# Kernel optimization log

Hardware: AMD Instinct MI355X
Metric: run time of the kernel (lower is better)

Reference implementation:

```python
import jax, jax.numpy as jnp
import numpy as np

N_NODES = 100000
N_EDGES = 600000
PRE = 128
NEXT = 128


def setup_inputs() -> dict:
    key = jax.random.key(0)
    k1, k2, k3, k4, k5, k6 = jax.random.split(key, 6)
    node_embedding = jax.random.normal(k1, (N_NODES, PRE), dtype=jnp.float32)
    edges = jax.random.randint(k2, (N_EDGES, 2), 0, N_NODES, dtype=jnp.int64)
    # Linear weights use torch convention [out, in]; scale ~ He-ish for sanity.
    s = 1.0 / np.sqrt(PRE)
    W_left = jax.random.normal(k3, (NEXT, PRE), dtype=jnp.float32) * s
    W_right = jax.random.normal(k4, (NEXT, PRE), dtype=jnp.float32) * s
    W_update = jax.random.normal(k5, (NEXT, PRE), dtype=jnp.float32) * s
    b_update = jax.random.normal(k6, (NEXT,), dtype=jnp.float32) * s
    return {
        "node_embedding": node_embedding,
        "edges": edges,
        "W_left": W_left,
        "W_right": W_right,
        "W_update": W_update,
        "b_update": b_update,
        "next_size": NEXT,
    }


def reference(node_embedding, edges, W_left, W_right, W_update, b_update, next_size):
    # Vectorized form of the per-edge loop:
    #   for each edge (i0, i1):
    #     lg  = sigmoid(W_l @ x[i0])
    #     rg  = sigmoid(W_r @ x[i1])
    #     mid = tanh(W_u @ (x[i0] + x[i1]) + b)
    #     out = lg*mid + rg*mid
    x0 = node_embedding[edges[:, 0]]  # [E, pre]
    x1 = node_embedding[edges[:, 1]]  # [E, pre]
    lg = jax.nn.sigmoid(jnp.einsum("ep,np->en", x0, W_left))
    rg = jax.nn.sigmoid(jnp.einsum("ep,np->en", x1, W_right))
    mid = jnp.tanh(jnp.einsum("ep,np->en", x0 + x1, W_update) + b_update)
    return (lg + rg) * mid  # [E, next]
```

## Files before the change

kernel.cpp:

```cpp
#include <hip/hip_runtime.h>
#include <hip/hip_bf16.h>
#include <hip/hip_fp16.h>

typedef __attribute__((ext_vector_type(8))) short short8;
typedef __attribute__((ext_vector_type(4))) float f32x4;

__device__ __forceinline__ float bflo(unsigned int u) { return __uint_as_float(u << 16); }
__device__ __forceinline__ float bfhi(unsigned int u) { return __uint_as_float(u & 0xffff0000u); }
__device__ __forceinline__ unsigned int bfrne(float f) {
    unsigned int u = __float_as_uint(f);
    return (u + 0x7fffu + ((u >> 16) & 1u)) >> 16;
}
__device__ __forceinline__ unsigned int packbf2(float lo, float hi) {
    return (bfrne(lo) & 0xffffu) | (bfrne(hi) << 16);
}
__device__ __forceinline__ short8 pack8(const float* f) {
    short8 r;
#pragma unroll
    for (int i = 0; i < 8; i += 2) {
        unsigned int p = packbf2(f[i], f[i + 1]);
        r[i] = (short)(p & 0xffffu);
        r[i + 1] = (short)(p >> 16);
    }
    return r;
}
__device__ __forceinline__ void unpackbf8(uint4 v, float* f) {
    const unsigned int* p = (const unsigned int*)&v;
#pragma unroll
    for (int j = 0; j < 4; ++j) { f[2 * j] = bflo(p[j]); f[2 * j + 1] = bfhi(p[j]); }
}

__device__ __forceinline__ unsigned int packh2(float lo, float hi) {
    unsigned int a = __half_as_ushort(__float2half_rn(lo));
    unsigned int b = __half_as_ushort(__float2half_rn(hi));
    return a | (b << 16);
}
__device__ __forceinline__ void unpackh8(uint4 v, float* f) {
    const unsigned int* p = (const unsigned int*)&v;
#pragma unroll
    for (int j = 0; j < 4; ++j) {
        f[2 * j]     = __half2float(__ushort_as_half((unsigned short)(p[j] & 0xffffu)));
        f[2 * j + 1] = __half2float(__ushort_as_half((unsigned short)(p[j] >> 16)));
    }
}

__device__ __forceinline__ float fast_rcp(float x) { return __builtin_amdgcn_rcpf(x); }
__device__ __forceinline__ float sigmoidf_fast(float x) { return fast_rcp(1.0f + __expf(-x)); }
__device__ __forceinline__ float tanhf_fast(float x) {
    float e = __expf(2.0f * x);
    return 1.0f - 2.0f * fast_rcp(e + 1.0f);
}

__global__ void sniff_kernel(const unsigned short* __restrict__ emb,
                             const int* __restrict__ e32, int* __restrict__ flags)
{
    __shared__ int s_f32, s_nz;
    const int t = threadIdx.x;
    if (t == 0) { s_f32 = 0; s_nz = 0; }
    __syncthreads();
    int bad = 0;
#pragma unroll 4
    for (int j = 0; j < 64; ++j) {
        unsigned int u = emb[t * 64 + j];
        if (((u >> 7) & 0xFFu) == 0xFFu) bad = 1;
    }
    int nz = 0;
#pragma unroll
    for (int j = 0; j < 8; ++j)
        if (e32[(t * 8 + j) * 2 + 1] != 0) nz = 1;
    if (bad) atomicOr(&s_f32, 1);
    if (nz) atomicOr(&s_nz, 1);
    __syncthreads();
    if (t == 0) { flags[0] = s_f32; flags[1] = s_nz ? 0 : 1; }
}

__global__ __launch_bounds__(256)
void prep_kernel(const void* __restrict__ w0v, const void* __restrict__ w1v,
                 const void* __restrict__ w2v,
                 unsigned short* __restrict__ Wb, const int* __restrict__ flags)
{
    const int in_f32 = flags[0];
    const int w = blockIdx.x;
    const void* Wv = (w == 0) ? w0v : (w == 1 ? w1v : w2v);
    unsigned short* dst = Wb + w * 16384;
    const int tid = threadIdx.x;
    if (in_f32) {
        const float* W = (const float*)Wv;
#pragma unroll
        for (int it = 0; it < 8; ++it) {
            int i = (tid + it * 256) * 8;
            float f[8];
            *(uint4*)&f[0] = *(const uint4*)(W + i);
            *(uint4*)&f[4] = *(const uint4*)(W + i + 4);
            *(short8*)(dst + i) = pack8(f);
        }
    } else {
        const unsigned short* W = (const unsigned short*)Wv;
#pragma unroll
        for (int it = 0; it < 8; ++it) {
            int i = (tid + it * 256) * 8;
            *(uint4*)(dst + i) = *(const uint4*)(W + i);
        }
    }
}

__global__ __launch_bounds__(256, 2)
void proj_kernel(const void* __restrict__ embv,
                 const unsigned short* __restrict__ Wb,
                 unsigned short* __restrict__ SLp,
                 unsigned short* __restrict__ SRp,
                 unsigned short* __restrict__ Up,
                 const int* __restrict__ flags, int n_nodes)
{
    const int in_f32 = flags[0];
    const int m0 = blockIdx.x * 128;

    __shared__ unsigned short ldsh[128 * 136];
    __shared__ unsigned short ldsl[128 * 136];

    const int tid  = threadIdx.x;
    const int lane = tid & 63;
    const int wave = tid >> 6;
    const int wm   = wave & 1;
    const int wn   = wave >> 1;
    const int l15  = lane & 15;
    const int lgp  = lane >> 4;

    if (in_f32) {
        const float* emb = (const float*)embv;
#pragma unroll
        for (int it = 0; it < 8; ++it) {
            int i = tid + it * 256;
            int row = i >> 4, ch = i & 15;
            int g = m0 + row;
            float f[8] = {0.f, 0.f, 0.f, 0.f, 0.f, 0.f, 0.f, 0.f};
            if (g < n_nodes) {
                const float* src = emb + (size_t)g * 128 + ch * 8;
                *(uint4*)&f[0] = *(const uint4*)src;
                *(uint4*)&f[4] = *(const uint4*)(src + 4);
            }
            short8 h, l;
#pragma unroll
            for (int j = 0; j < 8; ++j) {
                unsigned int uh = bfrne(f[j]);
                h[j] = (short)uh;
                float r = f[j] - __uint_as_float(uh << 16);
                l[j] = (short)bfrne(r);
            }
            *(short8*)(&ldsh[row * 136 + ch * 8]) = h;
            *(short8*)(&ldsl[row * 136 + ch * 8]) = l;
        }
    } else {
        const unsigned short* emb = (const unsigned short*)embv;
#pragma unroll
        for (int it = 0; it < 4; ++it) {
            int i = tid + it * 256;
            int row = i >> 3, ch = i & 7;
            int g = m0 + row;
            uint4 v = make_uint4(0u, 0u, 0u, 0u);
            if (g < n_nodes) v = *(const uint4*)(emb + (size_t)g * 128 + ch * 8);
            *(uint4*)(&ldsh[row * 136 + ch * 8]) = v;
        }
    }

    __syncthreads();

#pragma unroll 1
    for (int w = 0; w < 3; ++w) {
        const unsigned short* Wp = Wb + w * 16384;

        short8 bf[4][4];
#pragma unroll
        for (int nj = 0; nj < 4; ++nj) {
            const unsigned short* wrow = Wp + (size_t)(wn * 64 + nj * 16 + l15) * 128 + lgp * 8;
#pragma unroll
            for (int s = 0; s < 4; ++s)
                bf[s][nj] = *(const short8*)(wrow + s * 32);
        }

        f32x4 acc[4][4];
#pragma unroll
        for (int mi = 0; mi < 4; ++mi)
#pragma unroll
            for (int nj = 0; nj < 4; ++nj)
                acc[mi][nj] = (f32x4){0.f, 0.f, 0.f, 0.f};

#pragma unroll
        for (int s = 0; s < 4; ++s) {
            short8 afh[4];
#pragma unroll
            for (int mi = 0; mi < 4; ++mi)
                afh[mi] = *(const short8*)(&ldsh[(wm * 64 + mi * 16 + l15) * 136 + s * 32 + lgp * 8]);
#pragma unroll
            for (int mi = 0; mi < 4; ++mi)
#pragma unroll
                for (int nj = 0; nj < 4; ++nj)
                    acc[mi][nj] = __builtin_amdgcn_mfma_f32_16x16x32_bf16(
                        afh[mi], bf[s][nj], acc[mi][nj], 0, 0, 0);
            if (in_f32) {
                short8 afl[4];
#pragma unroll
                for (int mi = 0; mi < 4; ++mi)
                    afl[mi] = *(const short8*)(&ldsl[(wm * 64 + mi * 16 + l15) * 136 + s * 32 + lgp * 8]);
#pragma unroll
                for (int mi = 0; mi < 4; ++mi)
#pragma unroll
                    for (int nj = 0; nj < 4; ++nj)
                        acc[mi][nj] = __builtin_amdgcn_mfma_f32_16x16x32_bf16(
                            afl[mi], bf[s][nj], acc[mi][nj], 0, 0, 0);
            }
        }

        unsigned short* out = (w == 0) ? SLp : (w == 1 ? SRp : Up);
        const bool gate = (w < 2);
        const bool odd = (lane & 1);
#pragma unroll
        for (int mi = 0; mi < 4; ++mi) {
            int nodeBase = m0 + wm * 64 + mi * 16 + lgp * 4;
#pragma unroll
            for (int nj = 0; nj < 4; ++nj) {
                float v0 = acc[mi][nj][0];
                float v1 = acc[mi][nj][1];
                float v2 = acc[mi][nj][2];
                float v3 = acc[mi][nj][3];
                if (gate) {
                    v0 = sigmoidf_fast(v0); v1 = sigmoidf_fast(v1);
                    v2 = sigmoidf_fast(v2); v3 = sigmoidf_fast(v3);
                }
                float p0 = __shfl_xor(v0, 1), p1 = __shfl_xor(v1, 1);
                float p2 = __shfl_xor(v2, 1), p3 = __shfl_xor(v3, 1);
                unsigned int pkA, pkB; int rA, rB;
                if (!odd) { pkA = packh2(v0, p0); rA = 0; pkB = packh2(v1, p1); rB = 1; }
                else      { pkA = packh2(p2, v2); rA = 2; pkB = packh2(p3, v3); rB = 3; }
                int colE = wn * 64 + nj * 16 + (l15 & ~1);
                int na = nodeBase + rA, nb = nodeBase + rB;
                if (na < n_nodes) *(unsigned int*)(out + (size_t)na * 128 + colE) = pkA;
                if (nb < n_nodes) *(unsigned int*)(out + (size_t)nb * 128 + colE) = pkB;
            }
        }
    }
}

__global__ __launch_bounds__(256)
void edge_kernel(const int* __restrict__ e32,
                 const unsigned short* __restrict__ SL,
                 const unsigned short* __restrict__ SR,
                 const unsigned short* __restrict__ U,
                 const void* __restrict__ biasv,
                 void* __restrict__ outv,
                 const int* __restrict__ flags, int n_edges)
{
    const int in_f32 = flags[0];
    const int i64    = flags[1];
    const int tid = threadIdx.x;
    const int e = blockIdx.x * 16 + (tid >> 4);
    if (e >= n_edges) return;
    const int c = (tid & 15) * 8;

    int a, b;
    if (i64) { int4 ev = *(const int4*)(e32 + 4 * (size_t)e); a = ev.x; b = ev.z; }
    else     { int2 ev = *(const int2*)(e32 + 2 * (size_t)e); a = ev.x; b = ev.y; }

    float slf[8], srf[8], uaf[8], ubf[8], bif[8];
    unpackh8(*(const uint4*)(SL + (size_t)a * 128 + c), slf);
    unpackh8(*(const uint4*)(SR + (size_t)b * 128 + c), srf);
    unpackh8(*(const uint4*)(U  + (size_t)a * 128 + c), uaf);
    unpackh8(*(const uint4*)(U  + (size_t)b * 128 + c), ubf);
    if (in_f32) {
        const float* bp = (const float*)biasv + c;
        *(uint4*)&bif[0] = *(const uint4*)bp;
        *(uint4*)&bif[4] = *(const uint4*)(bp + 4);
    } else {
        unpackbf8(*(const uint4*)((const unsigned short*)biasv + c), bif);
    }

    float o[8];
#pragma unroll
    for (int j = 0; j < 8; ++j) {
        float s = slf[j] + srf[j];
        float x = uaf[j] + ubf[j] + bif[j];
        o[j] = s * tanhf_fast(x);
    }

    if (in_f32) {
        float* op = (float*)outv + (size_t)e * 128 + c;
        *(uint4*)op = *(const uint4*)&o[0];
        *(uint4*)(op + 4) = *(const uint4*)&o[4];
    } else {
        unsigned int res[4];
#pragma unroll
        for (int j = 0; j < 4; ++j) res[j] = packbf2(o[2 * j], o[2 * j + 1]);
        *(uint4*)((unsigned short*)outv + (size_t)e * 128 + c) = *(const uint4*)res;
    }
}

extern "C" void kernel_launch(void* const* d_in, const int* in_sizes, int n_in,
                              void* d_out, int out_size, void* d_ws, size_t ws_size,
                              hipStream_t stream)
{
    const void* emb   = d_in[0];
    const int*  edges = (const int*)d_in[1];
    const void* Wl    = d_in[2];
    const void* Wr    = d_in[3];
    const void* Wu    = d_in[4];
    const void* bias  = d_in[5];

    const int n_nodes = in_sizes[0] / 128;
    const int n_edges = in_sizes[1] / 2;

    int* flags = (int*)d_ws;
    unsigned short* Wb = (unsigned short*)((char*)d_ws + 256);
    const size_t plane_elems = (size_t)n_nodes * 128;
    unsigned short* SLp = Wb + 3 * 16384;
    unsigned short* SRp = SLp + plane_elems;
    unsigned short* Up  = SRp + plane_elems;

    sniff_kernel<<<1, 256, 0, stream>>>((const unsigned short*)emb, edges, flags);

    prep_kernel<<<3, 256, 0, stream>>>(Wl, Wr, Wu, Wb, flags);

    dim3 g1((n_nodes + 127) / 128);
    proj_kernel<<<g1, 256, 0, stream>>>(emb, Wb, SLp, SRp, Up, flags, n_nodes);

    int g2 = (n_edges + 15) / 16;
    edge_kernel<<<g2, 256, 0, stream>>>(edges, SLp, SRp, Up, bias, d_out, flags, n_edges);
}
```

Before: 475.7 us.

## Quantize gate projections to uint8, fold bias into U, merge sniff into prep

```diff
diff --git a/kernel.cpp b/kernel.cpp
--- a/kernel.cpp
+++ b/kernel.cpp
@@ -4,6 +4,10 @@
 
 typedef __attribute__((ext_vector_type(8))) short short8;
 typedef __attribute__((ext_vector_type(4))) float f32x4;
+typedef __attribute__((ext_vector_type(4))) unsigned int u32x4;
+typedef __attribute__((ext_vector_type(2))) unsigned int u32x2;
+typedef __attribute__((ext_vector_type(4))) int i32x4;
+typedef __attribute__((ext_vector_type(2))) int i32x2;
 
 __device__ __forceinline__ float bflo(unsigned int u) { return __uint_as_float(u << 16); }
 __device__ __forceinline__ float bfhi(unsigned int u) { return __uint_as_float(u & 0xffff0000u); }
@@ -24,23 +28,17 @@
     }
     return r;
 }
-__device__ __forceinline__ void unpackbf8(uint4 v, float* f) {
-    const unsigned int* p = (const unsigned int*)&v;
-#pragma unroll
-    for (int j = 0; j < 4; ++j) { f[2 * j] = bflo(p[j]); f[2 * j + 1] = bfhi(p[j]); }
-}
 
 __device__ __forceinline__ unsigned int packh2(float lo, float hi) {
     unsigned int a = __half_as_ushort(__float2half_rn(lo));
     unsigned int b = __half_as_ushort(__float2half_rn(hi));
     return a | (b << 16);
 }
-__device__ __forceinline__ void unpackh8(uint4 v, float* f) {
-    const unsigned int* p = (const unsigned int*)&v;
+__device__ __forceinline__ void unpackh8(u32x4 v, float* f) {
 #pragma unroll
     for (int j = 0; j < 4; ++j) {
-        f[2 * j]     = __half2float(__ushort_as_half((unsigned short)(p[j] & 0xffffu)));
-        f[2 * j + 1] = __half2float(__ushort_as_half((unsigned short)(p[j] >> 16)));
+        f[2 * j]     = __half2float(__ushort_as_half((unsigned short)(v[j] & 0xffffu)));
+        f[2 * j + 1] = __half2float(__ushort_as_half((unsigned short)(v[j] >> 16)));
     }
 }
 
@@ -51,8 +49,13 @@
     return 1.0f - 2.0f * fast_rcp(e + 1.0f);
 }
 
-__global__ void sniff_kernel(const unsigned short* __restrict__ emb,
-                             const int* __restrict__ e32, int* __restrict__ flags)
+__global__ __launch_bounds__(256)
+void prep_kernel(const void* __restrict__ w0v, const void* __restrict__ w1v,
+                 const void* __restrict__ w2v,
+                 unsigned short* __restrict__ Wb,
+                 const unsigned short* __restrict__ emb16,
+                 const int* __restrict__ e32,
+                 int* __restrict__ flags)
 {
     __shared__ int s_f32, s_nz;
     const int t = threadIdx.x;
@@ -61,7 +64,7 @@
     int bad = 0;
 #pragma unroll 4
     for (int j = 0; j < 64; ++j) {
-        unsigned int u = emb[t * 64 + j];
+        unsigned int u = emb16[t * 64 + j];
         if (((u >> 7) & 0xFFu) == 0xFFu) bad = 1;
     }
     int nz = 0;
@@ -71,35 +74,28 @@
     if (bad) atomicOr(&s_f32, 1);
     if (nz) atomicOr(&s_nz, 1);
     __syncthreads();
-    if (t == 0) { flags[0] = s_f32; flags[1] = s_nz ? 0 : 1; }
-}
-
-__global__ __launch_bounds__(256)
-void prep_kernel(const void* __restrict__ w0v, const void* __restrict__ w1v,
-                 const void* __restrict__ w2v,
-                 unsigned short* __restrict__ Wb, const int* __restrict__ flags)
-{
-    const int in_f32 = flags[0];
+    const int in_f32 = s_f32;
+    if (blockIdx.x == 0 && t == 0) { flags[0] = in_f32; flags[1] = s_nz ? 0 : 1; }
+
     const int w = blockIdx.x;
     const void* Wv = (w == 0) ? w0v : (w == 1 ? w1v : w2v);
     unsigned short* dst = Wb + w * 16384;
-    const int tid = threadIdx.x;
     if (in_f32) {
         const float* W = (const float*)Wv;
 #pragma unroll
         for (int it = 0; it < 8; ++it) {
-            int i = (tid + it * 256) * 8;
+            int i = (t + it * 256) * 8;
             float f[8];
-            *(uint4*)&f[0] = *(const uint4*)(W + i);
-            *(uint4*)&f[4] = *(const uint4*)(W + i + 4);
+            *(u32x4*)&f[0] = *(const u32x4*)(W + i);
+            *(u32x4*)&f[4] = *(const u32x4*)(W + i + 4);
             *(short8*)(dst + i) = pack8(f);
         }
     } else {
         const unsigned short* W = (const unsigned short*)Wv;
 #pragma unroll
         for (int it = 0; it < 8; ++it) {
-            int i = (tid + it * 256) * 8;
-            *(uint4*)(dst + i) = *(const uint4*)(W + i);
+            int i = (t + it * 256) * 8;
+            *(u32x4*)(dst + i) = *(const u32x4*)(W + i);
         }
     }
 }
@@ -107,9 +103,10 @@
 __global__ __launch_bounds__(256, 2)
 void proj_kernel(const void* __restrict__ embv,
                  const unsigned short* __restrict__ Wb,
-                 unsigned short* __restrict__ SLp,
-                 unsigned short* __restrict__ SRp,
+                 unsigned char* __restrict__ SLp,
+                 unsigned char* __restrict__ SRp,
                  unsigned short* __restrict__ Up,
+                 const void* __restrict__ biasv,
                  const int* __restrict__ flags, int n_nodes)
 {
     const int in_f32 = flags[0];
@@ -136,8 +133,8 @@
             float f[8] = {0.f, 0.f, 0.f, 0.f, 0.f, 0.f, 0.f, 0.f};
             if (g < n_nodes) {
                 const float* src = emb + (size_t)g * 128 + ch * 8;
-                *(uint4*)&f[0] = *(const uint4*)src;
-                *(uint4*)&f[4] = *(const uint4*)(src + 4);
+                *(u32x4*)&f[0] = __builtin_nontemporal_load((const u32x4*)src);
+                *(u32x4*)&f[4] = __builtin_nontemporal_load((const u32x4*)(src + 4));
             }
             short8 h, l;
 #pragma unroll
@@ -157,9 +154,9 @@
             int i = tid + it * 256;
             int row = i >> 3, ch = i & 7;
             int g = m0 + row;
-            uint4 v = make_uint4(0u, 0u, 0u, 0u);
-            if (g < n_nodes) v = *(const uint4*)(emb + (size_t)g * 128 + ch * 8);
-            *(uint4*)(&ldsh[row * 136 + ch * 8]) = v;
+            u32x4 v = (u32x4){0u, 0u, 0u, 0u};
+            if (g < n_nodes) v = *(const u32x4*)(emb + (size_t)g * 128 + ch * 8);
+            *(u32x4*)(&ldsh[row * 136 + ch * 8]) = v;
         }
     }
 
@@ -211,31 +208,63 @@
             }
         }
 
-        unsigned short* out = (w == 0) ? SLp : (w == 1 ? SRp : Up);
-        const bool gate = (w < 2);
         const bool odd = (lane & 1);
-#pragma unroll
-        for (int mi = 0; mi < 4; ++mi) {
-            int nodeBase = m0 + wm * 64 + mi * 16 + lgp * 4;
-#pragma unroll
-            for (int nj = 0; nj < 4; ++nj) {
-                float v0 = acc[mi][nj][0];
-                float v1 = acc[mi][nj][1];
-                float v2 = acc[mi][nj][2];
-                float v3 = acc[mi][nj][3];
-                if (gate) {
-                    v0 = sigmoidf_fast(v0); v1 = sigmoidf_fast(v1);
-                    v2 = sigmoidf_fast(v2); v3 = sigmoidf_fast(v3);
+        if (w < 2) {
+            unsigned char* out8 = (w == 0) ? SLp : SRp;
+#pragma unroll
+            for (int mi = 0; mi < 4; ++mi) {
+                int nodeBase = m0 + wm * 64 + mi * 16 + lgp * 4;
+#pragma unroll
+                for (int nj = 0; nj < 4; ++nj) {
+                    unsigned int q0 = (unsigned int)(sigmoidf_fast(acc[mi][nj][0]) * 255.f + 0.5f);
+                    unsigned int q1 = (unsigned int)(sigmoidf_fast(acc[mi][nj][1]) * 255.f + 0.5f);
+                    unsigned int q2 = (unsigned int)(sigmoidf_fast(acc[mi][nj][2]) * 255.f + 0.5f);
+                    unsigned int q3 = (unsigned int)(sigmoidf_fast(acc[mi][nj][3]) * 255.f + 0.5f);
+                    unsigned int p0 = (unsigned int)__shfl_xor((int)q0, 1);
+                    unsigned int p1 = (unsigned int)__shfl_xor((int)q1, 1);
+                    unsigned int p2 = (unsigned int)__shfl_xor((int)q2, 1);
+                    unsigned int p3 = (unsigned int)__shfl_xor((int)q3, 1);
+                    unsigned int hA, hB;
+                    if (!odd) { hA = q0 | (p0 << 8); hB = q1 | (p1 << 8); }
+                    else      { hA = p2 | (q2 << 8); hB = p3 | (q3 << 8); }
+                    unsigned int mA = (unsigned int)__shfl_xor((int)hA, 2);
+                    unsigned int mB = (unsigned int)__shfl_xor((int)hB, 2);
+                    unsigned int wordA = (l15 & 2) ? (mA | (hA << 16)) : (hA | (mA << 16));
+                    unsigned int wordB = (l15 & 2) ? (mB | (hB << 16)) : (hB | (mB << 16));
+                    int sel = l15 & 3;
+                    int r = (sel & 1) * 2 + (sel >> 1);
+                    unsigned int word = (sel >> 1) ? wordB : wordA;
+                    int node = nodeBase + r;
+                    int colB = wn * 64 + nj * 16 + (l15 & ~3);
+                    if (node < n_nodes)
+                        *(unsigned int*)(out8 + (size_t)node * 128 + colB) = word;
                 }
-                float p0 = __shfl_xor(v0, 1), p1 = __shfl_xor(v1, 1);
-                float p2 = __shfl_xor(v2, 1), p3 = __shfl_xor(v3, 1);
-                unsigned int pkA, pkB; int rA, rB;
-                if (!odd) { pkA = packh2(v0, p0); rA = 0; pkB = packh2(v1, p1); rB = 1; }
-                else      { pkA = packh2(p2, v2); rA = 2; pkB = packh2(p3, v3); rB = 3; }
-                int colE = wn * 64 + nj * 16 + (l15 & ~1);
-                int na = nodeBase + rA, nb = nodeBase + rB;
-                if (na < n_nodes) *(unsigned int*)(out + (size_t)na * 128 + colE) = pkA;
-                if (nb < n_nodes) *(unsigned int*)(out + (size_t)nb * 128 + colE) = pkB;
+            }
+        } else {
+            const float* bias_f = (const float*)biasv;
+            const unsigned short* bias_h = (const unsigned short*)biasv;
+#pragma unroll
+            for (int mi = 0; mi < 4; ++mi) {
+                int nodeBase = m0 + wm * 64 + mi * 16 + lgp * 4;
+#pragma unroll
+                for (int nj = 0; nj < 4; ++nj) {
+                    int col = wn * 64 + nj * 16 + l15;
+                    float bv = 0.5f * (in_f32 ? bias_f[col]
+                                              : __uint_as_float(((unsigned int)bias_h[col]) << 16));
+                    float v0 = acc[mi][nj][0] + bv;
+                    float v1 = acc[mi][nj][1] + bv;
+                    float v2 = acc[mi][nj][2] + bv;
+                    float v3 = acc[mi][nj][3] + bv;
+                    float p0 = __shfl_xor(v0, 1), p1 = __shfl_xor(v1, 1);
+                    float p2 = __shfl_xor(v2, 1), p3 = __shfl_xor(v3, 1);
+                    unsigned int pkA, pkB; int rA, rB;
+                    if (!odd) { pkA = packh2(v0, p0); rA = 0; pkB = packh2(v1, p1); rB = 1; }
+                    else      { pkA = packh2(p2, v2); rA = 2; pkB = packh2(p3, v3); rB = 3; }
+                    int colE = wn * 64 + nj * 16 + (l15 & ~1);
+                    int na = nodeBase + rA, nb = nodeBase + rB;
+                    if (na < n_nodes) *(unsigned int*)(Up + (size_t)na * 128 + colE) = pkA;
+                    if (nb < n_nodes) *(unsigned int*)(Up + (size_t)nb * 128 + colE) = pkB;
+                }
             }
         }
     }
@@ -243,10 +272,9 @@
 
 __global__ __launch_bounds__(256)
 void edge_kernel(const int* __restrict__ e32,
-                 const unsigned short* __restrict__ SL,
-                 const unsigned short* __restrict__ SR,
+                 const unsigned char* __restrict__ SL,
+                 const unsigned char* __restrict__ SR,
                  const unsigned short* __restrict__ U,
-                 const void* __restrict__ biasv,
                  void* __restrict__ outv,
                  const int* __restrict__ flags, int n_edges)
 {
@@ -258,39 +286,38 @@
     const int c = (tid & 15) * 8;
 
     int a, b;
-    if (i64) { int4 ev = *(const int4*)(e32 + 4 * (size_t)e); a = ev.x; b = ev.z; }
-    else     { int2 ev = *(const int2*)(e32 + 2 * (size_t)e); a = ev.x; b = ev.y; }
-
-    float slf[8], srf[8], uaf[8], ubf[8], bif[8];
-    unpackh8(*(const uint4*)(SL + (size_t)a * 128 + c), slf);
-    unpackh8(*(const uint4*)(SR + (size_t)b * 128 + c), srf);
-    unpackh8(*(const uint4*)(U  + (size_t)a * 128 + c), uaf);
-    unpackh8(*(const uint4*)(U  + (size_t)b * 128 + c), ubf);
-    if (in_f32) {
-        const float* bp = (const float*)biasv + c;
-        *(uint4*)&bif[0] = *(const uint4*)bp;
-        *(uint4*)&bif[4] = *(const uint4*)(bp + 4);
-    } else {
-        unpackbf8(*(const uint4*)((const unsigned short*)biasv + c), bif);
-    }
-
+    if (i64) { i32x4 ev = __builtin_nontemporal_load((const i32x4*)(e32 + 4 * (size_t)e)); a = ev[0]; b = ev[2]; }
+    else     { i32x2 ev = __builtin_nontemporal_load((const i32x2*)(e32 + 2 * (size_t)e)); a = ev[0]; b = ev[1]; }
+
+    u32x2 qla = *(const u32x2*)(SL + (size_t)a * 128 + c);
+    u32x2 qrb = *(const u32x2*)(SR + (size_t)b * 128 + c);
+    float uaf[8], ubf[8];
+    unpackh8(*(const u32x4*)(U + (size_t)a * 128 + c), uaf);
+    unpackh8(*(const u32x4*)(U + (size_t)b * 128 + c), ubf);
+
+    const float inv255 = 1.f / 255.f;
     float o[8];
 #pragma unroll
-    for (int j = 0; j < 8; ++j) {
-        float s = slf[j] + srf[j];
-        float x = uaf[j] + ubf[j] + bif[j];
-        o[j] = s * tanhf_fast(x);
+    for (int j = 0; j < 4; ++j) {
+        float s = (float)(((qla[0] >> (8 * j)) & 255u) + ((qrb[0] >> (8 * j)) & 255u)) * inv255;
+        o[j] = s * tanhf_fast(uaf[j] + ubf[j]);
+    }
+#pragma unroll
+    for (int j = 0; j < 4; ++j) {
+        float s = (float)(((qla[1] >> (8 * j)) & 255u) + ((qrb[1] >> (8 * j)) & 255u)) * inv255;
+        o[4 + j] = s * tanhf_fast(uaf[4 + j] + ubf[4 + j]);
     }
 
     if (in_f32) {
         float* op = (float*)outv + (size_t)e * 128 + c;
-        *(uint4*)op = *(const uint4*)&o[0];
-        *(uint4*)(op + 4) = *(const uint4*)&o[4];
+        __builtin_nontemporal_store(*(const u32x4*)&o[0], (u32x4*)op);
+        __builtin_nontemporal_store(*(const u32x4*)&o[4], (u32x4*)(op + 4));
     } else {
         unsigned int res[4];
 #pragma unroll
         for (int j = 0; j < 4; ++j) res[j] = packbf2(o[2 * j], o[2 * j + 1]);
-        *(uint4*)((unsigned short*)outv + (size_t)e * 128 + c) = *(const uint4*)res;
+        __builtin_nontemporal_store(*(const u32x4*)res,
+                                    (u32x4*)((unsigned short*)outv + (size_t)e * 128 + c));
     }
 }
 
@@ -310,18 +337,16 @@
 
     int* flags = (int*)d_ws;
     unsigned short* Wb = (unsigned short*)((char*)d_ws + 256);
-    const size_t plane_elems = (size_t)n_nodes * 128;
-    unsigned short* SLp = Wb + 3 * 16384;
-    unsigned short* SRp = SLp + plane_elems;
-    unsigned short* Up  = SRp + plane_elems;
-
-    sniff_kernel<<<1, 256, 0, stream>>>((const unsigned short*)emb, edges, flags);
-
-    prep_kernel<<<3, 256, 0, stream>>>(Wl, Wr, Wu, Wb, flags);
+    unsigned char* SLp = (unsigned char*)(Wb + 3 * 16384);
+    unsigned char* SRp = SLp + (size_t)n_nodes * 128;
+    unsigned short* Up = (unsigned short*)(SRp + (size_t)n_nodes * 128);
+
+    prep_kernel<<<3, 256, 0, stream>>>(Wl, Wr, Wu, Wb,
+                                       (const unsigned short*)emb, edges, flags);
 
     dim3 g1((n_nodes + 127) / 128);
-    proj_kernel<<<g1, 256, 0, stream>>>(emb, Wb, SLp, SRp, Up, flags, n_nodes);
+    proj_kernel<<<g1, 256, 0, stream>>>(emb, Wb, SLp, SRp, Up, bias, flags, n_nodes);
 
     int g2 = (n_edges + 15) / 16;
-    edge_kernel<<<g2, 256, 0, stream>>>(edges, SLp, SRp, Up, bias, d_out, flags, n_edges);
-}
+    edge_kernel<<<g2, 256, 0, stream>>>(edges, SLp, SRp, Up, d_out, flags, n_edges);
+}
```

New measurement: 470.8 us (median of 2 runs). About the same (-1.0%).
